# Kernel tuning notes

Measured on AMD Instinct MI355X. Metric: run time of the kernel, lower is better.

Reference implementation:

```python
import jax, jax.numpy as jnp
import numpy as np

N, K, D = 1000000, 8, 32


def setup_inputs() -> dict:
    key = jax.random.key(0)
    k_x, k_mu, k_phi = jax.random.split(key, 3)
    X = jax.random.normal(k_x, (N, D), dtype=jnp.float32)
    # Gaussian.__init__: mu = (rand(dims) - 0.5) * 2, sigma = eye(dims)
    mus = (jax.random.uniform(k_mu, (K, D), dtype=jnp.float32) - 0.5) * 2.0
    sigmas = jnp.broadcast_to(jnp.eye(D, dtype=jnp.float32), (K, D, D)).copy()
    # GMM.__init__: phi ~ Dirichlet(1/count); approximate with normalized uniforms
    phi_raw = jax.random.uniform(k_phi, (K,), dtype=jnp.float32) + 1e-3
    phis = phi_raw / phi_raw.sum()
    return {"X": X, "mus": mus, "sigmas": sigmas, "phis": phis}


def reference(X, mus, sigmas, phis):
    # X: [N, D], mus: [K, D], sigmas: [K, D, D], phis: [K]
    d = X.shape[1]
    inv_sigma = jnp.linalg.pinv(sigmas)                      # [K, D, D]
    _, logdet = jnp.linalg.slogdet(sigmas)                   # [K]
    log_two_pi_dims = d * jnp.log(jnp.asarray(2.0 * np.pi, dtype=X.dtype))
    log_den = 0.5 * (log_two_pi_dims + logdet)               # [K]
    diff = X[:, None, :] - mus[None, :, :]                   # [N, K, D]
    # batched Mahalanobis quadratic form: -0.5 * diff @ inv_sigma @ diff^T (diag)
    quad = -0.5 * jnp.einsum('nkd,kde,nke->nk', diff, inv_sigma, diff)  # [N, K]
    # original subtracts exp(log_den), then scales by phi per mixture
    aff = phis[None, :] * (quad - jnp.exp(log_den)[None, :])  # [N, K]
    # ExpNormalizer.exp_norm == row-wise softmax
    return jax.nn.softmax(aff, axis=1)
```

## Files before the change

kernel.cpp:

```cpp
#include <hip/hip_runtime.h>
#include <hip/hip_bf16.h>
#include <math.h>

#define DDIM 32
#define KMIX 8
#define TPW 5

typedef short bf16x8 __attribute__((ext_vector_type(8)));
typedef float f32x4 __attribute__((ext_vector_type(4)));

__device__ __forceinline__ ushort to_bf16_rne(float f) {
    unsigned u = __builtin_bit_cast(unsigned, f);
    u = (u + 0x7FFFu + ((u >> 16) & 1u)) >> 16;
    return (ushort)u;
}

__global__ __launch_bounds__(1024) void gmm_prep(
    const float* __restrict__ S, const float* __restrict__ mus,
    const float* __restrict__ phis, ushort* __restrict__ Wtg,
    ushort* __restrict__ Upan, float* __restrict__ pa2, float* __restrict__ pc)
{
    __shared__ float aug[DDIM][2 * DDIM + 2];
    __shared__ float ch[DDIM][DDIM + 1];
    __shared__ float pivsave[DDIM];
    __shared__ float amuL[DDIM];
    __shared__ float logL[DDIM];
    const int k = blockIdx.x;
    const int t = threadIdx.x;
    const int r = t >> 5, c = t & 31;

    aug[r][c]      = S[k * 1024 + r * 32 + c];
    aug[r][c + 32] = (c == r) ? 1.f : 0.f;
    __syncthreads();

    for (int p = 0; p < DDIM; ++p) {
        const float piv   = aug[p][p];
        const float f     = aug[r][p];
        const float prow  = aug[p][c];
        const float prow2 = aug[p][c + 32];
        __syncthreads();
        const float ip = 1.f / piv;
        if (r == p) {
            aug[r][c]      = prow * ip;
            aug[r][c + 32] = prow2 * ip;
            if (c == 0) pivsave[p] = piv;
        } else {
            const float fi = f * ip;
            aug[r][c]      = fmaf(-fi, prow,  aug[r][c]);
            aug[r][c + 32] = fmaf(-fi, prow2, aug[r][c + 32]);
        }
        __syncthreads();
    }

    if (t < DDIM) {
        float acc = 0.f;
        for (int d = 0; d < DDIM; ++d)
            acc = fmaf(aug[t][32 + d], mus[k * 32 + d], acc);
        amuL[t] = acc;
        logL[t] = logf(fabsf(pivsave[t]));
    }
    ch[r][c] = aug[r][32 + c];
    __syncthreads();

    for (int j = 0; j < DDIM; ++j) {
        const float djj = ch[j][j];
        const float cr  = ch[r][j];
        const float cc  = ch[c][j];
        __syncthreads();
        if (c == j) {
            ch[r][j] = (r >= j) ? cr * rsqrtf(djj) : 0.f;
        } else if (r > j && c > j) {
            ch[r][c] = fmaf(-cr * __builtin_amdgcn_rcpf(djj), cc, ch[r][c]);
        }
        __syncthreads();
    }

    {
        const int h    = t >> 9;
        const int lane = (t >> 3) & 63;
        const int j    = t & 7;
        const int d = (lane >> 4) * 8 + j;
        const int e = h * 16 + (lane & 15);
        const float fv = (d >= e) ? ch[d][e] : 0.f;
        Wtg[k * 1024 + t] = to_bf16_rne(fv);
    }
    if (t < DDIM)
        Upan[k * 32 + t] = to_bf16_rne(phis[k] * 1.4426950408889634f * amuL[t]);
    if (k == 0 && t >= 256 && t < 512) Upan[t] = 0;
    if (t == 0) {
        float ldet = 0.f, muAmu = 0.f;
        for (int i = 0; i < DDIM; ++i) {
            ldet += logL[i];
            muAmu = fmaf(amuL[i], mus[k * 32 + i], muAmu);
        }
        const float eld = expf(0.5f * (DDIM * 1.8378770664093453f + ldet));
        const float LOG2E = 1.4426950408889634f;
        pa2[k] = -0.5f * phis[k] * LOG2E;
        pc[k]  = (-0.5f * phis[k] * muAmu - phis[k] * eld) * LOG2E;
    }
}

template <int CTRL>
__device__ __forceinline__ float dpp_add(float v) {
    int t = __builtin_amdgcn_update_dpp(0, __builtin_bit_cast(int, v), CTRL, 0xF, 0xF, true);
    return v + __builtin_bit_cast(float, t);
}
template <int CTRL>
__device__ __forceinline__ float dpp_max(float v) {
    int t = __builtin_amdgcn_update_dpp(0, __builtin_bit_cast(int, v), CTRL, 0xF, 0xF, true);
    return fmaxf(v, __builtin_bit_cast(float, t));
}
__device__ __forceinline__ float sel4(float a0, float a1, float a2, float a3, int r) {
    float b0 = (r & 1) ? a1 : a0;
    float b1 = (r & 1) ? a3 : a2;
    return (r & 2) ? b1 : b0;
}
__device__ __forceinline__ float bperm_f(int addr, float v) {
    return __builtin_bit_cast(float, __builtin_amdgcn_ds_bpermute(addr, __builtin_bit_cast(int, v)));
}

__global__ __launch_bounds__(256, 6) void gmm_main(
    const float* __restrict__ X, const ushort* __restrict__ Wtg,
    const ushort* __restrict__ Upan, const float* __restrict__ pa2g,
    const float* __restrict__ pcg, float* __restrict__ out, int N)
{
    __shared__ ushort wtab[KMIX * 1024];
    const int tid = threadIdx.x;
    const int lane = tid & 63;
    const int wid = tid >> 6;
    const int g = lane >> 4;
    const int c = lane & 15;
    const int rsel = c & 3;
    const int r1 = g * 4 + rsel;
    const int p = c >> 2;

    {
        const float4* src = (const float4*)Wtg;
        float4* dst = (float4*)wtab;
#pragma unroll
        for (int i = 0; i < 4; ++i) dst[tid + 256 * i] = src[tid + 256 * i];
    }

    const bf16x8 uf = *(const bf16x8*)(Upan + c * 32 + g * 8);
    const float paA = pa2g[2 * p], paB = pa2g[2 * p + 1];
    const float pcA = pcg[2 * p],  pcB = pcg[2 * p + 1];
    const int src_byte = (((p >> 1) * 16 + r1) << 2);

    const int ntiles = N >> 4;
    const int tile0 = (blockIdx.x * 4 + wid) * TPW;
    const float* lp = X + (size_t)tile0 * 512 + c * 32 + g * 8;
    float* op = out + (size_t)(tile0 * 16 + r1) * 8 + p * 2;

    const f32x4 zro = {0.f, 0.f, 0.f, 0.f};
    float4 a0 = {0,0,0,0}, a1 = {0,0,0,0};
    if (tile0 < ntiles) { a0 = *(const float4*)lp; a1 = *(const float4*)(lp + 4); }

    __syncthreads();

#pragma unroll
    for (int it = 0; it < TPW; ++it) {
        const int tile = tile0 + it;
        float4 b0 = a0, b1 = a1;
        if (it + 1 < TPW && tile + 1 < ntiles) {
            b0 = *(const float4*)(lp + 512);
            b1 = *(const float4*)(lp + 516);
        }
        if (tile < ntiles) {
            int4 xi;
            xi.x = __builtin_amdgcn_perm(__builtin_bit_cast(unsigned, a0.y), __builtin_bit_cast(unsigned, a0.x), 0x07060302u);
            xi.y = __builtin_amdgcn_perm(__builtin_bit_cast(unsigned, a0.w), __builtin_bit_cast(unsigned, a0.z), 0x07060302u);
            xi.z = __builtin_amdgcn_perm(__builtin_bit_cast(unsigned, a1.y), __builtin_bit_cast(unsigned, a1.x), 0x07060302u);
            xi.w = __builtin_amdgcn_perm(__builtin_bit_cast(unsigned, a1.w), __builtin_bit_cast(unsigned, a1.z), 0x07060302u);
            const bf16x8 xf = __builtin_bit_cast(bf16x8, xi);

            const f32x4 lin = __builtin_amdgcn_mfma_f32_16x16x32_bf16(uf, xf, zro, 0, 0, 0);

            int la = lane * 16;
            asm volatile("" : "+v"(la));
            const char* wb = (const char*)wtab + la;

            float qa = 0.f, qb = 0.f;
#pragma unroll
            for (int k = 0; k < KMIX; ++k) {
                const bf16x8 wf0k = *(const bf16x8*)(wb + (k * 2 + 0) * 1024);
                const bf16x8 wf1k = *(const bf16x8*)(wb + (k * 2 + 1) * 1024);
                f32x4 acc0 = __builtin_amdgcn_mfma_f32_16x16x32_bf16(xf, wf0k, zro, 0, 0, 0);
                f32x4 acc1 = __builtin_amdgcn_mfma_f32_16x16x32_bf16(xf, wf1k, zro, 0, 0, 0);
                float p0 = fmaf(acc1[0], acc1[0], acc0[0] * acc0[0]);
                float p1 = fmaf(acc1[1], acc1[1], acc0[1] * acc0[1]);
                float p2 = fmaf(acc1[2], acc1[2], acc0[2] * acc0[2]);
                float p3 = fmaf(acc1[3], acc1[3], acc0[3] * acc0[3]);
                p0 = dpp_add<0xB1>(p0); p0 = dpp_add<0x4E>(p0);
                p1 = dpp_add<0xB1>(p1); p1 = dpp_add<0x4E>(p1);
                p2 = dpp_add<0xB1>(p2); p2 = dpp_add<0x4E>(p2);
                p3 = dpp_add<0xB1>(p3); p3 = dpp_add<0x4E>(p3);
                float v = sel4(p0, p1, p2, p3, rsel);
                v = dpp_add<0x124>(v);
                v = dpp_add<0x128>(v);
                if ((k >> 1) == 0) { if (p == 0) { if (k & 1) qb = v; else qa = v; } }
                if ((k >> 1) == 1) { if (p == 1) { if (k & 1) qb = v; else qa = v; } }
                if ((k >> 1) == 2) { if (p == 2) { if (k & 1) qb = v; else qa = v; } }
                if ((k >> 1) == 3) { if (p == 3) { if (k & 1) qb = v; else qa = v; } }
            }

            const float l0 = bperm_f(src_byte, lin[0]);
            const float l1 = bperm_f(src_byte, lin[1]);
            const float l2 = bperm_f(src_byte, lin[2]);
            const float l3 = bperm_f(src_byte, lin[3]);
            const float lina = (p & 1) ? l2 : l0;
            const float linb = (p & 1) ? l3 : l1;
            const float aka = fmaf(paA, qa, pcA) + lina;
            const float akb = fmaf(paB, qb, pcB) + linb;

            float m = fmaxf(aka, akb);
            m = dpp_max<0x124>(m); m = dpp_max<0x128>(m);
            const float ea = __builtin_amdgcn_exp2f(aka - m);
            const float eb = __builtin_amdgcn_exp2f(akb - m);
            float s = ea + eb;
            s = dpp_add<0x124>(s); s = dpp_add<0x128>(s);
            const float inv = __builtin_amdgcn_rcpf(s);
            *(float2*)op = make_float2(ea * inv, eb * inv);
        }
        a0 = b0; a1 = b1;
        lp += 512;
        op += 128;
    }
}

extern "C" void kernel_launch(void* const* d_in, const int* in_sizes, int n_in,
                              void* d_out, int out_size, void* d_ws, size_t ws_size,
                              hipStream_t stream) {
    const float* X    = (const float*)d_in[0];
    const float* mus  = (const float*)d_in[1];
    const float* sig  = (const float*)d_in[2];
    const float* phis = (const float*)d_in[3];
    float* out = (float*)d_out;

    float* ws    = (float*)d_ws;
    float* pa2   = ws;
    float* pc    = ws + 8;
    ushort* Upan = (ushort*)(ws + 16);
    ushort* Wtg  = (ushort*)(ws + 272);

    const int N = in_sizes[0] / DDIM;

    gmm_prep<<<KMIX, 1024, 0, stream>>>(sig, mus, phis, Wtg, Upan, pa2, pc);

    const int ntiles = N >> 4;
    const int grid = (ntiles + 4 * TPW - 1) / (4 * TPW);
    gmm_main<<<grid, 256, 0, stream>>>(X, Wtg, Upan, pa2, pc, out, N);
}
```

Baseline: 56.00 us.

## Rework GMM prep with LDL and Newton inverse, fold mean into quadratic

The prep kernel replaces Gauss-Jordan plus Cholesky with an LDL elimination and Newton–Schulz iterations that invert the unit-lower factor, using 256 threads instead of 1024. The main kernel drops the separate linear MFMA and bpermute path. It subtracts a precomputed L^-1 mu vector from the MFMA outputs before squaring, and replaces the per-row max reduction with a constant max of pc. TPW doubles so each wave handles more tiles. The fixed softmax shift assumes the quadratic terms stay bounded (pa2 is negative, so exponents stay at or below zero), and fewer blocks may reduce latency hiding.

```diff
diff --git a/kernel.cpp b/kernel.cpp
--- a/kernel.cpp
+++ b/kernel.cpp
@@ -4,7 +4,7 @@
 
 #define DDIM 32
 #define KMIX 8
-#define TPW 5
+#define TPW 10
 
 typedef short bf16x8 __attribute__((ext_vector_type(8)));
 typedef float f32x4 __attribute__((ext_vector_type(4)));
@@ -15,88 +15,102 @@
     return (ushort)u;
 }
 
-__global__ __launch_bounds__(1024) void gmm_prep(
+__global__ __launch_bounds__(256) void gmm_prep(
     const float* __restrict__ S, const float* __restrict__ mus,
     const float* __restrict__ phis, ushort* __restrict__ Wtg,
-    ushort* __restrict__ Upan, float* __restrict__ pa2, float* __restrict__ pc)
+    float* __restrict__ wvec, float* __restrict__ pa2, float* __restrict__ pc)
 {
-    __shared__ float aug[DDIM][2 * DDIM + 2];
-    __shared__ float ch[DDIM][DDIM + 1];
-    __shared__ float pivsave[DDIM];
-    __shared__ float amuL[DDIM];
-    __shared__ float logL[DDIM];
+    __shared__ float A[DDIM][DDIM + 1];
+    __shared__ float V0[DDIM][DDIM + 1];
+    __shared__ float V1[DDIM][DDIM + 1];
+    __shared__ float T[DDIM][DDIM + 1];
+    __shared__ float pivd[DDIM], irt[DDIM], muL[DDIM];
     const int k = blockIdx.x;
     const int t = threadIdx.x;
-    const int r = t >> 5, c = t & 31;
-
-    aug[r][c]      = S[k * 1024 + r * 32 + c];
-    aug[r][c + 32] = (c == r) ? 1.f : 0.f;
+    const int r = t >> 3;
+    const int c0 = t & 7;
+
+#pragma unroll
+    for (int i = 0; i < 4; ++i) {
+        const int c = c0 + 8 * i;
+        A[r][c]  = S[k * 1024 + r * 32 + c];
+        V0[r][c] = (r == c) ? 1.f : 0.f;
+        V1[r][c] = 0.f;
+    }
+    if (t < DDIM) muL[t] = mus[k * 32 + t];
     __syncthreads();
 
     for (int p = 0; p < DDIM; ++p) {
-        const float piv   = aug[p][p];
-        const float f     = aug[r][p];
-        const float prow  = aug[p][c];
-        const float prow2 = aug[p][c + 32];
-        __syncthreads();
-        const float ip = 1.f / piv;
-        if (r == p) {
-            aug[r][c]      = prow * ip;
-            aug[r][c + 32] = prow2 * ip;
-            if (c == 0) pivsave[p] = piv;
-        } else {
-            const float fi = f * ip;
-            aug[r][c]      = fmaf(-fi, prow,  aug[r][c]);
-            aug[r][c + 32] = fmaf(-fi, prow2, aug[r][c + 32]);
-        }
-        __syncthreads();
-    }
+        const float piv = A[p][p];
+        const float fr  = A[r][p];
+        float prow[4];
+#pragma unroll
+        for (int i = 0; i < 4; ++i) prow[i] = A[p][c0 + 8 * i];
+        __syncthreads();
+        const float fi = fr * __builtin_amdgcn_rcpf(piv);
+        if (r > p) {
+#pragma unroll
+            for (int i = 0; i < 4; ++i) {
+                const int c = c0 + 8 * i;
+                if (c > p)       A[r][c] = fmaf(-fi, prow[i], A[r][c]);
+                else if (c == p) A[r][c] = fi;
+            }
+        }
+        if (t == (p << 3)) pivd[p] = piv;
+        __syncthreads();
+    }
+
+    auto newton = [&](float (*Vc)[DDIM + 1], float (*Vn)[DDIM + 1]) {
+#pragma unroll
+        for (int i = 0; i < 4; ++i) {
+            const int c = c0 + 8 * i;
+            if (c <= r) {
+                float s = Vc[r][c];
+                for (int j = c; j < r; ++j) s = fmaf(A[r][j], Vc[j][c], s);
+                T[r][c] = s;
+            }
+        }
+        __syncthreads();
+#pragma unroll
+        for (int i = 0; i < 4; ++i) {
+            const int c = c0 + 8 * i;
+            if (c <= r) {
+                float s = 0.f;
+                for (int j = c; j <= r; ++j) s = fmaf(Vc[r][j], T[j][c], s);
+                Vn[r][c] = fmaf(2.f, Vc[r][c], -s);
+            }
+        }
+        __syncthreads();
+    };
+    newton(V0, V1); newton(V1, V0); newton(V0, V1); newton(V1, V0); newton(V0, V1);
 
     if (t < DDIM) {
-        float acc = 0.f;
-        for (int d = 0; d < DDIM; ++d)
-            acc = fmaf(aug[t][32 + d], mus[k * 32 + d], acc);
-        amuL[t] = acc;
-        logL[t] = logf(fabsf(pivsave[t]));
-    }
-    ch[r][c] = aug[r][32 + c];
+        irt[t] = rsqrtf(pivd[t]);
+        float z = 0.f;
+        for (int j = 0; j <= t; ++j) z = fmaf(V1[t][j], muL[j], z);
+        wvec[k * 32 + t] = z * rsqrtf(pivd[t]);
+    }
     __syncthreads();
 
-    for (int j = 0; j < DDIM; ++j) {
-        const float djj = ch[j][j];
-        const float cr  = ch[r][j];
-        const float cc  = ch[c][j];
-        __syncthreads();
-        if (c == j) {
-            ch[r][j] = (r >= j) ? cr * rsqrtf(djj) : 0.f;
-        } else if (r > j && c > j) {
-            ch[r][c] = fmaf(-cr * __builtin_amdgcn_rcpf(djj), cc, ch[r][c]);
-        }
-        __syncthreads();
-    }
-
-    {
-        const int h    = t >> 9;
-        const int lane = (t >> 3) & 63;
-        const int j    = t & 7;
+#pragma unroll
+    for (int rep = 0; rep < 4; ++rep) {
+        const int i = t + 256 * rep;
+        const int h = i >> 9, lane = (i >> 3) & 63, j = i & 7;
         const int d = (lane >> 4) * 8 + j;
         const int e = h * 16 + (lane & 15);
-        const float fv = (d >= e) ? ch[d][e] : 0.f;
-        Wtg[k * 1024 + t] = to_bf16_rne(fv);
-    }
-    if (t < DDIM)
-        Upan[k * 32 + t] = to_bf16_rne(phis[k] * 1.4426950408889634f * amuL[t]);
-    if (k == 0 && t >= 256 && t < 512) Upan[t] = 0;
-    if (t == 0) {
-        float ldet = 0.f, muAmu = 0.f;
-        for (int i = 0; i < DDIM; ++i) {
-            ldet += logL[i];
-            muAmu = fmaf(amuL[i], mus[k * 32 + i], muAmu);
-        }
-        const float eld = expf(0.5f * (DDIM * 1.8378770664093453f + ldet));
-        const float LOG2E = 1.4426950408889634f;
-        pa2[k] = -0.5f * phis[k] * LOG2E;
-        pc[k]  = (-0.5f * phis[k] * muAmu - phis[k] * eld) * LOG2E;
+        const float fv = (e >= d) ? V1[e][d] * irt[e] : 0.f;
+        Wtg[k * 1024 + i] = to_bf16_rne(fv);
+    }
+
+    if (t < 64) {
+        float l = (t < DDIM) ? logf(pivd[t]) : 0.f;
+        for (int off = 32; off; off >>= 1) l += __shfl_xor(l, off, 64);
+        if (t == 0) {
+            const float eld = expf(0.5f * (DDIM * 1.8378770664093453f + l));
+            const float LOG2E = 1.4426950408889634f;
+            pa2[k] = -0.5f * phis[k] * LOG2E;
+            pc[k]  = -phis[k] * eld * LOG2E;
+        }
     }
 }
 
@@ -105,23 +119,15 @@
     int t = __builtin_amdgcn_update_dpp(0, __builtin_bit_cast(int, v), CTRL, 0xF, 0xF, true);
     return v + __builtin_bit_cast(float, t);
 }
-template <int CTRL>
-__device__ __forceinline__ float dpp_max(float v) {
-    int t = __builtin_amdgcn_update_dpp(0, __builtin_bit_cast(int, v), CTRL, 0xF, 0xF, true);
-    return fmaxf(v, __builtin_bit_cast(float, t));
-}
 __device__ __forceinline__ float sel4(float a0, float a1, float a2, float a3, int r) {
     float b0 = (r & 1) ? a1 : a0;
     float b1 = (r & 1) ? a3 : a2;
     return (r & 2) ? b1 : b0;
 }
-__device__ __forceinline__ float bperm_f(int addr, float v) {
-    return __builtin_bit_cast(float, __builtin_amdgcn_ds_bpermute(addr, __builtin_bit_cast(int, v)));
-}
 
 __global__ __launch_bounds__(256, 6) void gmm_main(
     const float* __restrict__ X, const ushort* __restrict__ Wtg,
-    const ushort* __restrict__ Upan, const float* __restrict__ pa2g,
+    const float* __restrict__ wvec, const float* __restrict__ pa2g,
     const float* __restrict__ pcg, float* __restrict__ out, int N)
 {
     __shared__ ushort wtab[KMIX * 1024];
@@ -141,10 +147,18 @@
         for (int i = 0; i < 4; ++i) dst[tid + 256 * i] = src[tid + 256 * i];
     }
 
-    const bf16x8 uf = *(const bf16x8*)(Upan + c * 32 + g * 8);
+    float nw0[KMIX], nw1[KMIX];
+#pragma unroll
+    for (int k = 0; k < KMIX; ++k) {
+        nw0[k] = -wvec[k * 32 + c];
+        nw1[k] = -wvec[k * 32 + 16 + c];
+    }
+    float pcv0 = pcg[0], pcv1 = pcg[1], pcv2 = pcg[2], pcv3 = pcg[3];
+    float pcv4 = pcg[4], pcv5 = pcg[5], pcv6 = pcg[6], pcv7 = pcg[7];
+    const float m8 = fmaxf(fmaxf(fmaxf(pcv0, pcv1), fmaxf(pcv2, pcv3)),
+                           fmaxf(fmaxf(pcv4, pcv5), fmaxf(pcv6, pcv7)));
     const float paA = pa2g[2 * p], paB = pa2g[2 * p + 1];
-    const float pcA = pcg[2 * p],  pcB = pcg[2 * p + 1];
-    const int src_byte = (((p >> 1) * 16 + r1) << 2);
+    const float pcsA = pcg[2 * p] - m8, pcsB = pcg[2 * p + 1] - m8;
 
     const int ntiles = N >> 4;
     const int tile0 = (blockIdx.x * 4 + wid) * TPW;
@@ -173,8 +187,6 @@
             xi.w = __builtin_amdgcn_perm(__builtin_bit_cast(unsigned, a1.w), __builtin_bit_cast(unsigned, a1.z), 0x07060302u);
             const bf16x8 xf = __builtin_bit_cast(bf16x8, xi);
 
-            const f32x4 lin = __builtin_amdgcn_mfma_f32_16x16x32_bf16(uf, xf, zro, 0, 0, 0);
-
             int la = lane * 16;
             asm volatile("" : "+v"(la));
             const char* wb = (const char*)wtab + la;
@@ -182,14 +194,20 @@
             float qa = 0.f, qb = 0.f;
 #pragma unroll
             for (int k = 0; k < KMIX; ++k) {
-                const bf16x8 wf0k = *(const bf16x8*)(wb + (k * 2 + 0) * 1024);
+                bf16x8 wf0k = {0, 0, 0, 0, 0, 0, 0, 0};
+                if (lane < 32)
+                    wf0k = *(const bf16x8*)(wb + (k * 2 + 0) * 1024);
                 const bf16x8 wf1k = *(const bf16x8*)(wb + (k * 2 + 1) * 1024);
                 f32x4 acc0 = __builtin_amdgcn_mfma_f32_16x16x32_bf16(xf, wf0k, zro, 0, 0, 0);
                 f32x4 acc1 = __builtin_amdgcn_mfma_f32_16x16x32_bf16(xf, wf1k, zro, 0, 0, 0);
-                float p0 = fmaf(acc1[0], acc1[0], acc0[0] * acc0[0]);
-                float p1 = fmaf(acc1[1], acc1[1], acc0[1] * acc0[1]);
-                float p2 = fmaf(acc1[2], acc1[2], acc0[2] * acc0[2]);
-                float p3 = fmaf(acc1[3], acc1[3], acc0[3] * acc0[3]);
+                const float d00 = acc0[0] + nw0[k], d10 = acc1[0] + nw1[k];
+                const float d01 = acc0[1] + nw0[k], d11 = acc1[1] + nw1[k];
+                const float d02 = acc0[2] + nw0[k], d12 = acc1[2] + nw1[k];
+                const float d03 = acc0[3] + nw0[k], d13 = acc1[3] + nw1[k];
+                float p0 = fmaf(d10, d10, d00 * d00);
+                float p1 = fmaf(d11, d11, d01 * d01);
+                float p2 = fmaf(d12, d12, d02 * d02);
+                float p3 = fmaf(d13, d13, d03 * d03);
                 p0 = dpp_add<0xB1>(p0); p0 = dpp_add<0x4E>(p0);
                 p1 = dpp_add<0xB1>(p1); p1 = dpp_add<0x4E>(p1);
                 p2 = dpp_add<0xB1>(p2); p2 = dpp_add<0x4E>(p2);
@@ -203,19 +221,10 @@
                 if ((k >> 1) == 3) { if (p == 3) { if (k & 1) qb = v; else qa = v; } }
             }
 
-            const float l0 = bperm_f(src_byte, lin[0]);
-            const float l1 = bperm_f(src_byte, lin[1]);
-            const float l2 = bperm_f(src_byte, lin[2]);
-            const float l3 = bperm_f(src_byte, lin[3]);
-            const float lina = (p & 1) ? l2 : l0;
-            const float linb = (p & 1) ? l3 : l1;
-            const float aka = fmaf(paA, qa, pcA) + lina;
-            const float akb = fmaf(paB, qb, pcB) + linb;
-
-            float m = fmaxf(aka, akb);
-            m = dpp_max<0x124>(m); m = dpp_max<0x128>(m);
-            const float ea = __builtin_amdgcn_exp2f(aka - m);
-            const float eb = __builtin_amdgcn_exp2f(akb - m);
+            const float aka = fmaf(paA, qa, pcsA);
+            const float akb = fmaf(paB, qb, pcsB);
+            const float ea = __builtin_amdgcn_exp2f(aka);
+            const float eb = __builtin_amdgcn_exp2f(akb);
             float s = ea + eb;
             s = dpp_add<0x124>(s); s = dpp_add<0x128>(s);
             const float inv = __builtin_amdgcn_rcpf(s);
@@ -239,14 +248,14 @@
     float* ws    = (float*)d_ws;
     float* pa2   = ws;
     float* pc    = ws + 8;
-    ushort* Upan = (ushort*)(ws + 16);
+    float* wvec  = ws + 16;
     ushort* Wtg  = (ushort*)(ws + 272);
 
     const int N = in_sizes[0] / DDIM;
-
-    gmm_prep<<<KMIX, 1024, 0, stream>>>(sig, mus, phis, Wtg, Upan, pa2, pc);
-
     const int ntiles = N >> 4;
+
+    gmm_prep<<<KMIX, 256, 0, stream>>>(sig, mus, phis, Wtg, wvec, pa2, pc);
+
     const int grid = (ntiles + 4 * TPW - 1) / (4 * TPW);
-    gmm_main<<<grid, 256, 0, stream>>>(X, Wtg, Upan, pa2, pc, out, N);
-}
+    gmm_main<<<grid, 256, 0, stream>>>(X, Wtg, wvec, pa2, pc, out, N);
+}
```

After: 90.42 us. 61.5% more time.
